# Performance work log

Hardware: AMD Instinct MI355X
Metric: run time of the kernel (lower is better)

Reference implementation:

```python
import jax, jax.numpy as jnp
import numpy as np
from jax import lax

H_IMG = 224
NUM_HEADS = 8
EPS = 1e-5


def setup_inputs() -> dict:
    key = jax.random.key(0)
    ks = jax.random.split(key, 16)
    C, Dff = 256, 512
    conv_s = 1.0 / np.sqrt(C * 9)
    lin_s = 1.0 / np.sqrt(C)
    lin2_s = 1.0 / np.sqrt(Dff)
    inp = {
        'lidar': jax.random.normal(ks[0], (2, C, H_IMG, H_IMG), jnp.float32),
        'image': jax.random.normal(ks[1], (2, C, H_IMG, H_IMG), jnp.float32),
        'cl_w': jax.random.normal(ks[2], (C, C, 3, 3), jnp.float32) * conv_s,
        'cl_b': jnp.zeros((C,), jnp.float32),
        'bnl_g': jnp.ones((C,), jnp.float32), 'bnl_b': jnp.zeros((C,), jnp.float32),
        'bnl_m': jnp.zeros((C,), jnp.float32), 'bnl_v': jnp.ones((C,), jnp.float32),
        'ci_w': jax.random.normal(ks[3], (C, C, 3, 3), jnp.float32) * conv_s,
        'ci_b': jnp.zeros((C,), jnp.float32),
        'bni_g': jnp.ones((C,), jnp.float32), 'bni_b': jnp.zeros((C,), jnp.float32),
        'bni_m': jnp.zeros((C,), jnp.float32), 'bni_v': jnp.ones((C,), jnp.float32),
        'qw': jax.random.normal(ks[4], (C, C), jnp.float32) * lin_s,
        'qb': jnp.zeros((C,), jnp.float32),
        'kw': jax.random.normal(ks[5], (C, C), jnp.float32) * lin_s,
        'kb': jnp.zeros((C,), jnp.float32),
        'vw': jax.random.normal(ks[6], (C, C), jnp.float32) * lin_s,
        'vb': jnp.zeros((C,), jnp.float32),
        'ow': jax.random.normal(ks[7], (C, C), jnp.float32) * lin_s,
        'ob': jnp.zeros((C,), jnp.float32),
        'ln1_g': jnp.ones((C,), jnp.float32), 'ln1_b': jnp.zeros((C,), jnp.float32),
        'w1': jax.random.normal(ks[8], (C, Dff), jnp.float32) * lin_s,
        'b1': jnp.zeros((Dff,), jnp.float32),
        'w2': jax.random.normal(ks[9], (Dff, C), jnp.float32) * lin2_s,
        'b2': jnp.zeros((C,), jnp.float32),
        'ln2_g': jnp.ones((C,), jnp.float32), 'ln2_b': jnp.zeros((C,), jnp.float32),
        'op_w': jax.random.normal(ks[10], (C, C, 1, 1), jnp.float32) * lin_s,
        'op_b': jnp.zeros((C,), jnp.float32),
        'sp_w': jax.random.normal(ks[11], (C, C, 1, 1), jnp.float32) * lin_s,
        'sp_b': jnp.zeros((C,), jnp.float32),
    }
    return inp


def _conv(x, w, b, stride, pad):
    y = lax.conv_general_dilated(x, w, (stride, stride), ((pad, pad), (pad, pad)),
                                 dimension_numbers=('NCHW', 'OIHW', 'NCHW'))
    return y + b[None, :, None, None]


def _bn(x, g, b, m, v):  # eval-mode BatchNorm2d
    inv = g * lax.rsqrt(v + EPS)
    return x * inv[None, :, None, None] + (b - m * inv)[None, :, None, None]


def _ln(x, g, b):
    mu = jnp.mean(x, -1, keepdims=True)
    var = jnp.mean(jnp.square(x - mu), -1, keepdims=True)
    return (x - mu) * lax.rsqrt(var + EPS) * g + b


def reference(lidar, image, cl_w, cl_b, bnl_g, bnl_b, bnl_m, bnl_v,
              ci_w, ci_b, bni_g, bni_b, bni_m, bni_v,
              qw, qb, kw, kb, vw, vb, ow, ob, ln1_g, ln1_b,
              w1, b1, w2, b2, ln2_g, ln2_b, op_w, op_b, sp_w, sp_b):
    B, C, H, W = lidar.shape
    # spatial compression (stride-4 conv + BN + ReLU)
    lc = jax.nn.relu(_bn(_conv(lidar, cl_w, cl_b, 4, 1), bnl_g, bnl_b, bnl_m, bnl_v))
    ic = jax.nn.relu(_bn(_conv(image, ci_w, ci_b, 4, 1), bni_g, bni_b, bni_m, bni_v))
    _, Ch, Hc, Wc = lc.shape
    N = Hc * Wc
    lseq = lc.reshape(B, Ch, N).transpose(0, 2, 1)  # (B,N,C)
    iseq = ic.reshape(B, Ch, N).transpose(0, 2, 1)

    # cross-attention (lidar queries, image keys/values)
    h, d = NUM_HEADS, Ch // NUM_HEADS
    scale = d ** -0.5
    Q = (lseq @ qw + qb).reshape(B, N, h, d).transpose(0, 2, 1, 3)
    K = (iseq @ kw + kb).reshape(B, N, h, d).transpose(0, 2, 1, 3)
    V = (iseq @ vw + vb).reshape(B, N, h, d).transpose(0, 2, 1, 3)
    scores = jnp.einsum('bhqd,bhkd->bhqk', Q, K) * scale
    attn = jax.nn.softmax(scores, axis=-1)
    ctx = jnp.einsum('bhqk,bhkd->bhqd', attn, V)
    attn_out = ctx.transpose(0, 2, 1, 3).reshape(B, N, Ch) @ ow + ob

    x = _ln(lseq + attn_out, ln1_g, ln1_b)
    ffn = jax.nn.relu(x @ w1 + b1) @ w2 + b2
    x = _ln(x + ffn, ln2_g, ln2_b)

    oc = x.transpose(0, 2, 1).reshape(B, Ch, Hc, Wc)
    up = jax.image.resize(oc, (B, Ch, H, W), method='bilinear')  # align_corners=False semantics
    out = _conv(up, op_w, op_b, 1, 0) + _conv(lidar, sp_w, sp_b, 1, 0)
    return out
```

## Files before the change

kernel.cpp:

```cpp
#include <hip/hip_runtime.h>
#include <hip/hip_bf16.h>

typedef __bf16 bf16;
typedef __attribute__((ext_vector_type(8))) __bf16 bf16x8;
typedef __attribute__((ext_vector_type(4))) __bf16 bf16x4;
typedef __attribute__((ext_vector_type(4))) float f32x4;
typedef __attribute__((ext_vector_type(4))) unsigned int u32x4;

#define LN_EPS 1e-5f

__device__ __forceinline__ void gload16(const void* g, void* l) {
  __builtin_amdgcn_global_load_lds(
      (__attribute__((address_space(1))) void*)g,
      (__attribute__((address_space(3))) void*)l, 16, 0, 0);
}

__device__ __forceinline__ unsigned pk2(float a, float b) {
  unsigned ua = __builtin_bit_cast(unsigned short, (bf16)a);
  unsigned ub = __builtin_bit_cast(unsigned short, (bf16)b);
  return ua | (ub << 16);
}

__device__ __forceinline__ float fexp2(float x) {
  float r;
  asm("v_exp_f32 %0, %1" : "=v"(r) : "v"(x));
  return r;
}


__global__ void bn_prep2_k(const float* cb0, const float* g0, const float* b0,
                           const float* m0, const float* v0, float* sc0, float* sh0,
                           const float* cb1, const float* g1, const float* b1,
                           const float* m1, const float* v1, float* sc1, float* sh1,
                           float* zp) {
  int c = threadIdx.x;
  bool z = blockIdx.x != 0;
  const float* cb = z ? cb1 : cb0;
  const float* g = z ? g1 : g0;
  const float* bb = z ? b1 : b0;
  const float* m = z ? m1 : m0;
  const float* v = z ? v1 : v0;
  float* sc = z ? sc1 : sc0;
  float* sh = z ? sh1 : sh0;
  float s = g[c] * rsqrtf(v[c] + LN_EPS);
  sc[c] = s;
  sh[c] = (cb[c] - m[c]) * s + bb[c];
  if (blockIdx.x == 0) zp[c] = 0.f;
}

__global__ void t_cvt4_k(const float* a0, const float* a1, const float* a2,
                         const float* a3, bf16* o0, bf16* o1, bf16* o2, bf16* o3) {
  __shared__ float tile[32][33];
  int z = blockIdx.z;
  const float* in = z == 0 ? a0 : z == 1 ? a1 : z == 2 ? a2 : a3;
  bf16* out = z == 0 ? o0 : z == 1 ? o1 : z == 2 ? o2 : o3;
  int c0 = blockIdx.x * 32, r0 = blockIdx.y * 32;
  int tx = threadIdx.x, ty = threadIdx.y;
  for (int yy = ty; yy < 32; yy += 8)
    tile[yy][tx] = in[(long)(r0 + yy) * 256 + c0 + tx];
  __syncthreads();
  for (int yy = ty; yy < 32; yy += 8)
    out[(long)(c0 + yy) * 256 + r0 + tx] = (bf16)tile[tx][yy];
}

__global__ void t_cvt_k(const float* __restrict__ in, bf16* __restrict__ out,
                        int R, int Cc) {
  __shared__ float tile[32][33];
  int c0 = blockIdx.x * 32, r0 = blockIdx.y * 32;
  int tx = threadIdx.x, ty = threadIdx.y;
  for (int yy = ty; yy < 32; yy += 8)
    tile[yy][tx] = in[(long)(r0 + yy) * Cc + c0 + tx];
  __syncthreads();
  for (int yy = ty; yy < 32; yy += 8)
    out[(long)(c0 + yy) * R + r0 + tx] = (bf16)tile[tx][yy];
}

__global__ void cvt2_k(const float* a0, const float* a1, bf16* o0, bf16* o1, int n) {
  const float* in = blockIdx.y ? a1 : a0;
  bf16* out = blockIdx.y ? o1 : o0;
  int i = (blockIdx.x * 256 + threadIdx.x) * 4;
  if (i < n) {
    float4 v = *(const float4*)(in + i);
    bf16x4 o = {(bf16)v.x, (bf16)v.y, (bf16)v.z, (bf16)v.w};
    *(bf16x4*)(out + i) = o;
  }
}

__global__ void wprep_k(const float* w0, const float* w1, bf16* o0, bf16* o1) {
  const float* w = blockIdx.y ? w1 : w0;
  bf16* o = blockIdx.y ? o1 : o0;
  int idx = blockIdx.x * 256 + threadIdx.x;
  int co = idx / 2304, r = idx - co * 2304;
  int k9 = r >> 8, ci = r & 255;
  o[idx] = (bf16)w[(co * 256 + ci) * 9 + k9];
}

__global__ __launch_bounds__(256) void t_in_k(const float* __restrict__ lid,
                                              const float* __restrict__ img,
                                              bf16* __restrict__ lidT,
                                              bf16* __restrict__ imgT) {
  int z = blockIdx.z;
  int b = z & 1;
  const float* in = (z < 2) ? lid : img;
  bf16* out = (z < 2) ? lidT : imgT;
  long p0 = (long)blockIdx.x * 64;
  int c0 = blockIdx.y * 64;
  __shared__ unsigned tile[64 * 36];
  int t = threadIdx.x;
  const float* ib = in + (long)b * 256 * 50176;
  bf16* ob = out + (long)b * 50176 * 256;
  int q = t & 15;
  int cp = t >> 4;
#pragma unroll
  for (int pp = 0; pp < 2; ++pp) {
    int ch = pp * 32 + cp * 2;
    const float* s = ib + (long)(c0 + ch) * 50176 + p0 + q * 4;
    float4 a = *(const float4*)s;
    float4 bv = *(const float4*)(s + 50176);
    unsigned wv[4] = {pk2(a.x, bv.x), pk2(a.y, bv.y), pk2(a.z, bv.z),
                      pk2(a.w, bv.w)};
    int g_log = pp * 4 + (cp >> 2);
    int colp = ((g_log ^ (q & 7)) << 2) | (cp & 3);
#pragma unroll
    for (int j = 0; j < 4; ++j)
      tile[(q * 4 + j) * 36 + colp] = wv[j];
  }
  __syncthreads();
  int px = t >> 3;
  int c8 = t & 7;
#pragma unroll
  for (int pp = 0; pp < 2; ++pp) {
    int p = pp * 32 + px;
    int colp = (c8 ^ ((p >> 2) & 7)) << 2;
    u32x4 vv = *(const u32x4*)&tile[p * 36 + colp];
    *(u32x4*)(ob + (p0 + p) * 256 + c0 + c8 * 8) = vv;
  }
}

__global__ void t_v_k(const bf16* __restrict__ V, bf16* __restrict__ Vt) {
  __shared__ bf16 tile[32][33];
  int b = blockIdx.z;
  int n0 = blockIdx.x * 32, c0 = blockIdx.y * 32;
  int tx = threadIdx.x, ty = threadIdx.y;
  for (int yy = ty; yy < 32; yy += 8)
    tile[yy][tx] = V[(long)(b * 3136 + n0 + yy) * 256 + c0 + tx];
  __syncthreads();
  for (int yy = ty; yy < 32; yy += 8)
    Vt[(long)(b * 256 + c0 + yy) * 3136 + n0 + tx] = tile[tx][yy];
}

__global__ void ln_k(const float* __restrict__ in, const float* __restrict__ g,
                     const float* __restrict__ bb, float* __restrict__ outf,
                     bf16* __restrict__ outb) {
  int w = threadIdx.x >> 6, l = threadIdx.x & 63;
  long row = (long)blockIdx.x * 4 + w;
  float4 v = *(const float4*)(in + row * 256 + l * 4);
  float s = v.x + v.y + v.z + v.w;
  for (int m = 1; m < 64; m <<= 1) s += __shfl_xor(s, m);
  float mu = s * (1.0f / 256.0f);
  float dx = v.x - mu, dy = v.y - mu, dz = v.z - mu, dw = v.w - mu;
  float q = dx * dx + dy * dy + dz * dz + dw * dw;
  for (int m = 1; m < 64; m <<= 1) q += __shfl_xor(q, m);
  float rstd = rsqrtf(q * (1.0f / 256.0f) + LN_EPS);
  int c = l * 4;
  float y0 = dx * rstd * g[c] + bb[c];
  float y1 = dy * rstd * g[c + 1] + bb[c + 1];
  float y2 = dz * rstd * g[c + 2] + bb[c + 2];
  float y3 = dw * rstd * g[c + 3] + bb[c + 3];
  if (outf) {
    float4 o = {y0, y1, y2, y3};
    *(float4*)(outf + row * 256 + c) = o;
  }
  bf16x4 ob = {(bf16)y0, (bf16)y1, (bf16)y2, (bf16)y3};
  *(bf16x4*)(outb + row * 256 + c) = ob;
}

__global__ __launch_bounds__(256) void upadd_k(float* __restrict__ out,
                                               const float* __restrict__ oc2T) {
  int id = blockIdx.x * 256 + threadIdx.x;
  int xq = id % 56;
  int rest = id / 56;
  int y = rest % 224;
  int rest2 = rest / 224;
  float4 v = *(float4*)(out + (long)id * 4);
  int ry = y & 3;
  int y0 = (y >> 2) - 1 + (ry >> 1);
  float wy = (ry == 0) ? 0.625f : (ry == 1) ? 0.875f : (ry == 2) ? 0.125f : 0.375f;
  int y0c = y0 > 0 ? y0 : 0, y1c = (y0 + 1) < 55 ? (y0 + 1) : 55;
  const float* base = oc2T + (long)rest2 * 3136;
  const float* r0 = base + y0c * 56;
  const float* r1 = base + y1c * 56;
  int xm = xq > 0 ? xq - 1 : 0;
  int xp = xq < 55 ? xq + 1 : 55;
  float a0 = r0[xm], a1 = r0[xq], a2 = r0[xp];
  float b0 = r1[xm], b1 = r1[xq], b2 = r1[xp];
  float t0 = 0.375f * a0 + 0.625f * a1;
  float t1 = 0.125f * a0 + 0.875f * a1;
  float t2 = 0.875f * a1 + 0.125f * a2;
  float t3 = 0.625f * a1 + 0.375f * a2;
  float u0 = 0.375f * b0 + 0.625f * b1;
  float u1 = 0.125f * b0 + 0.875f * b1;
  float u2 = 0.875f * b1 + 0.125f * b2;
  float u3 = 0.625f * b1 + 0.375f * b2;
  float iw = 1.f - wy;
  v.x += iw * t0 + wy * u0;
  v.y += iw * t1 + wy * u1;
  v.z += iw * t2 + wy * u2;
  v.w += iw * t3 + wy * u3;
  *(float4*)(out + (long)id * 4) = v;
}

struct ConvJob {
  const bf16* inT;
  const bf16* wT;
  const float* scale;
  const float* shift;
  bf16* out;
};

__global__ __launch_bounds__(256) void convgemm_k(ConvJob j0, ConvJob j1,
                                                  const bf16* zp) {
  const ConvJob jb = blockIdx.z ? j1 : j0;
  __shared__ bf16 lA[64 * 64];
  __shared__ bf16 lB[64 * 64];
  const int tid = threadIdx.x;
  const int w = tid >> 6, l = tid & 63;
  const int l15 = l & 15;
  const int m0 = blockIdx.x * 64;
  const int n0 = blockIdx.y * 64;
  const int mw = (w >> 1) * 32, nw = (w & 1) * 32;
  f32x4 acc[2][2] = {};
  const int srow = w * 8 + (l >> 3);
  const int kc8 = (l & 7) * 8;
  long rb[2];
  int voy[2], vox[2];
#pragma unroll
  for (int p = 0; p < 2; ++p) {
    int m = m0 + srow + p * 32;
    int b = m / 3136;
    int mm = m - b * 3136;
    int oy = mm / 56, ox = mm - oy * 56;
    rb[p] = ((long)b * 50176 + (long)(4 * oy - 1) * 224 + (4 * ox - 1)) * 256 + kc8;
    voy[p] = oy;
    vox[p] = ox;
  }
  const bf16* Bb = jb.wT + (long)(n0 + srow) * 2304 + kc8;
  bf16* lAp = &lA[srow * 64 + kc8];
  bf16* lBp = &lB[srow * 64 + kc8];
  const bf16* zsrc = zp + kc8;
#pragma unroll
  for (int st = 0; st < 36; ++st) {
    const int k9 = st >> 2, ci0 = (st & 3) * 64;
    const int ky = k9 / 3, kx = k9 - 3 * ky;
    const long koff = (long)(ky * 224 + kx) * 256 + ci0;
#pragma unroll
    for (int p = 0; p < 2; ++p) {
      bool ok = (voy[p] > 0 || ky > 0) && (vox[p] > 0 || kx > 0);
      const bf16* src = ok ? jb.inT + rb[p] + koff : zsrc;
      gload16(src, lAp + p * 32 * 64);
    }
    gload16(Bb + st * 64, lBp);
    gload16(Bb + 32 * 2304 + st * 64, lBp + 32 * 64);
    __syncthreads();
    const int kq = (l >> 4) * 8;
#pragma unroll
    for (int kk = 0; kk < 64; kk += 32) {
      bf16x8 af[2], bfv[2];
#pragma unroll
      for (int i = 0; i < 2; ++i)
        af[i] = *(const bf16x8*)&lA[(mw + i * 16 + l15) * 64 + kk + kq];
#pragma unroll
      for (int j = 0; j < 2; ++j)
        bfv[j] = *(const bf16x8*)&lB[(nw + j * 16 + l15) * 64 + kk + kq];
#pragma unroll
      for (int i = 0; i < 2; ++i)
#pragma unroll
        for (int j = 0; j < 2; ++j)
          acc[i][j] = __builtin_amdgcn_mfma_f32_16x16x32_bf16(af[i], bfv[j],
                                                              acc[i][j], 0, 0, 0);
    }
    __syncthreads();
  }
#pragma unroll
  for (int i = 0; i < 2; ++i)
#pragma unroll
    for (int j = 0; j < 2; ++j)
#pragma unroll
      for (int r = 0; r < 4; ++r) {
        const long row = m0 + mw + i * 16 + (l >> 4) * 4 + r;
        const long col = n0 + nw + j * 16 + l15;
        float v = fmaxf(acc[i][j][r] * jb.scale[col] + jb.shift[col], 0.f);
        jb.out[row * 256 + col] = (bf16)v;
      }
}


struct EpiParams {
  float* out0;
  bf16* out1;
  const float* v0;
  const float* res;
  const bf16* resb;
  int ldc;
  float mul;
};

struct GemmJob {
  const bf16* A;
  const bf16* Bt;
  EpiParams ep;
};

struct GemmJobs3 {
  GemmJob j[3];
};

enum { EPI_QKV = 0, EPI_BIAS_RELU_BF16 = 1, EPI_BIAS_ADD = 2,
       EPI_BIAS_ADDB = 3, EPI_ROWB_F32 = 4, EPI_SPADD = 5 };

template <int EPI, int BM, int BN>
__global__ __launch_bounds__(256) void gemm_bt(GemmJobs3 jobs, int K) {
  const GemmJob jb = jobs.j[blockIdx.z];
  const bf16* __restrict__ A = jb.A;
  const bf16* __restrict__ Bt = jb.Bt;
  const EpiParams ep = jb.ep;
  constexpr int MI = (BM == 128 && BN == 128) ? 4 : 2;
  constexpr int NJ = (BN == 128) ? 4 : 2;
  __shared__ bf16 lA[BM * 64];
  __shared__ bf16 lB[BN * 64];
  const int tid = threadIdx.x;
  const int w = tid >> 6, l = tid & 63;
  const int l15 = l & 15;
  const long m0 = (long)blockIdx.x * BM;
  const long n0 = (long)blockIdx.y * BN;
  const int mw = (BM == 128) ? ((BN == 128) ? (w >> 1) * 64 : w * 32)
                             : (w >> 1) * 32;
  const int nw = (BN == 128) ? (w & 1) * 64 : ((BM == 128) ? 0 : (w & 1) * 32);
  f32x4 acc[MI][NJ] = {};
  const int srow = w * 8 + (l >> 3);
  const int kc8 = (l & 7) * 8;
  const bf16* Ab = A + (m0 + srow) * (long)K + kc8;
  const bf16* Bb = Bt + (n0 + srow) * (long)K + kc8;
  bf16* lAp = &lA[srow * 64 + kc8];
  bf16* lBp = &lB[srow * 64 + kc8];
  for (int k0 = 0; k0 < K; k0 += 64) {
#pragma unroll
    for (int p = 0; p < BM / 32; ++p)
      gload16(Ab + (long)p * 32 * K + k0, lAp + p * 32 * 64);
#pragma unroll
    for (int p = 0; p < BN / 32; ++p)
      gload16(Bb + (long)p * 32 * K + k0, lBp + p * 32 * 64);
    __syncthreads();
    const int kq = (l >> 4) * 8;
#pragma unroll
    for (int kk = 0; kk < 64; kk += 32) {
      bf16x8 af[MI], bfv[NJ];
#pragma unroll
      for (int i = 0; i < MI; ++i)
        af[i] = *(const bf16x8*)&lA[(mw + i * 16 + l15) * 64 + kk + kq];
#pragma unroll
      for (int j = 0; j < NJ; ++j)
        bfv[j] = *(const bf16x8*)&lB[(nw + j * 16 + l15) * 64 + kk + kq];
#pragma unroll
      for (int i = 0; i < MI; ++i)
#pragma unroll
        for (int j = 0; j < NJ; ++j)
          acc[i][j] = __builtin_amdgcn_mfma_f32_16x16x32_bf16(af[i], bfv[j],
                                                              acc[i][j], 0, 0, 0);
    }
    __syncthreads();
  }
  const int ldc = ep.ldc;
#pragma unroll
  for (int i = 0; i < MI; ++i)
#pragma unroll
    for (int j = 0; j < NJ; ++j)
#pragma unroll
      for (int r = 0; r < 4; ++r) {
        const long row = m0 + mw + i * 16 + (l >> 4) * 4 + r;
        const long col = n0 + nw + j * 16 + l15;
        float v = acc[i][j][r];
        if constexpr (EPI == EPI_QKV) {
          ep.out1[row * ldc + col] = (bf16)((v + ep.v0[col]) * ep.mul);
        } else if constexpr (EPI == EPI_BIAS_RELU_BF16) {
          ep.out1[row * ldc + col] = (bf16)fmaxf(v + ep.v0[col], 0.f);
        } else if constexpr (EPI == EPI_BIAS_ADD) {
          ep.out0[row * ldc + col] = v + ep.v0[col] + ep.res[row * ldc + col];
        } else if constexpr (EPI == EPI_BIAS_ADDB) {
          ep.out0[row * ldc + col] =
              v + ep.v0[col] + (float)ep.resb[row * ldc + col];
        } else if constexpr (EPI == EPI_ROWB_F32) {
          ep.out0[row * ldc + col] = v + ep.v0[row];
        } else {
          ep.out0[row * ldc + col] = v + ep.v0[row];
        }
      }
}

__global__ __launch_bounds__(256) void flash_k(const bf16* __restrict__ Qg,
                                               const bf16* __restrict__ Kg,
                                               const bf16* __restrict__ Vt,
                                               bf16* __restrict__ ctx) {
  const int w = threadIdx.x >> 6, l = threadIdx.x & 63;
  const int fid = blockIdx.x;
  const int grp = (fid & 7) * 2 + ((fid >> 3) / 49);
  const int qt = (fid >> 3) % 49;
  const int b = grp >> 3, h = grp & 7;
  const int N = 3136;
  const int l15 = l & 15, g = l >> 4;
  const int q0 = (qt * 4 + w) * 16;
  const int kperm = 8 * (l15 >> 2) + (l15 & 3);
  __shared__ bf16 lds[2][4][512];

  bf16x8 qf = *(const bf16x8*)(Qg + ((long)(b * N + q0 + l15)) * 256 + h * 32 + g * 8);
  const bf16* Kb_ = Kg + ((long)b * N) * 256 + h * 32;
  const bf16* Vb_ = Vt + ((long)(b * 256 + h * 32)) * 3136;
  const long kOffA = (long)kperm * 256 + g * 8;
  const long kOffB = (long)(kperm + 4) * 256 + g * 8;
  const long vOff0 = (long)l15 * 3136 + g * 8;
  const long vOff1 = (long)(16 + l15) * 3136 + g * 8;

  f32x4 o0 = {}, o1 = {};
  float ls = 0.f;

  auto stage = [&](int buf, int kt) {
    const bf16* kp = Kb_ + (long)kt * 32 * 256;
    const bf16* vp = Vb_ + kt * 32;
    if (w == 0)
      gload16(kp + kOffA, &lds[buf][0][l * 8]);
    else if (w == 1)
      gload16(kp + kOffB, &lds[buf][1][l * 8]);
    else if (w == 2)
      gload16(vp + vOff0, &lds[buf][2][l * 8]);
    else
      gload16(vp + vOff1, &lds[buf][3][l * 8]);
  };

  stage(0, 0);
  __syncthreads();
  int cur = 0;
  for (int kt = 0; kt < 98; ++kt) {
    if (kt < 97) stage(cur ^ 1, kt + 1);
    bf16x8 kf0 = *(const bf16x8*)&lds[cur][0][l * 8];
    bf16x8 kf1 = *(const bf16x8*)&lds[cur][1][l * 8];
    bf16x8 vf0 = *(const bf16x8*)&lds[cur][2][l * 8];
    bf16x8 vf1 = *(const bf16x8*)&lds[cur][3][l * 8];
    f32x4 z = {};
    f32x4 s0 = __builtin_amdgcn_mfma_f32_16x16x32_bf16(kf0, qf, z, 0, 0, 0);
    f32x4 s1 = __builtin_amdgcn_mfma_f32_16x16x32_bf16(kf1, qf, z, 0, 0, 0);
    float p0 = fexp2(s0[0]), p1 = fexp2(s0[1]), p2 = fexp2(s0[2]), p3 = fexp2(s0[3]);
    float p4 = fexp2(s1[0]), p5 = fexp2(s1[1]), p6 = fexp2(s1[2]), p7 = fexp2(s1[3]);
    ls += ((p0 + p1) + (p2 + p3)) + ((p4 + p5) + (p6 + p7));
    u32x4 fp;
    fp[0] = pk2(p0, p1);
    fp[1] = pk2(p2, p3);
    fp[2] = pk2(p4, p5);
    fp[3] = pk2(p6, p7);
    bf16x8 pf = __builtin_bit_cast(bf16x8, fp);
    o0 = __builtin_amdgcn_mfma_f32_16x16x32_bf16(vf0, pf, o0, 0, 0, 0);
    o1 = __builtin_amdgcn_mfma_f32_16x16x32_bf16(vf1, pf, o1, 0, 0, 0);
    __syncthreads();
    cur ^= 1;
  }
  ls += __shfl_xor(ls, 16);
  ls += __shfl_xor(ls, 32);
  float inv = 1.0f / ls;
  long base = ((long)(b * N + q0 + l15)) * 256 + h * 32;
  bf16x4 ov0 = {(bf16)(o0[0] * inv), (bf16)(o0[1] * inv),
                (bf16)(o0[2] * inv), (bf16)(o0[3] * inv)};
  bf16x4 ov1 = {(bf16)(o1[0] * inv), (bf16)(o1[1] * inv),
                (bf16)(o1[2] * inv), (bf16)(o1[3] * inv)};
  *(bf16x4*)(ctx + base + g * 4) = ov0;
  *(bf16x4*)(ctx + base + 16 + g * 4) = ov1;
}


extern "C" void kernel_launch(void* const* d_in, const int* in_sizes, int n_in,
                              void* d_out, int out_size, void* d_ws, size_t ws_size,
                              hipStream_t stream) {
  const float* lidar = (const float*)d_in[0];
  const float* image = (const float*)d_in[1];
  const float* cl_w = (const float*)d_in[2];
  const float* cl_b = (const float*)d_in[3];
  const float* bnl_g = (const float*)d_in[4];
  const float* bnl_b = (const float*)d_in[5];
  const float* bnl_m = (const float*)d_in[6];
  const float* bnl_v = (const float*)d_in[7];
  const float* ci_w = (const float*)d_in[8];
  const float* ci_b = (const float*)d_in[9];
  const float* bni_g = (const float*)d_in[10];
  const float* bni_b = (const float*)d_in[11];
  const float* bni_m = (const float*)d_in[12];
  const float* bni_v = (const float*)d_in[13];
  const float* qw = (const float*)d_in[14];
  const float* qb = (const float*)d_in[15];
  const float* kw = (const float*)d_in[16];
  const float* kb = (const float*)d_in[17];
  const float* vw = (const float*)d_in[18];
  const float* vb = (const float*)d_in[19];
  const float* ow = (const float*)d_in[20];
  const float* ob = (const float*)d_in[21];
  const float* ln1_g = (const float*)d_in[22];
  const float* ln1_b = (const float*)d_in[23];
  const float* w1 = (const float*)d_in[24];
  const float* b1 = (const float*)d_in[25];
  const float* w2 = (const float*)d_in[26];
  const float* b2 = (const float*)d_in[27];
  const float* ln2_g = (const float*)d_in[28];
  const float* ln2_b = (const float*)d_in[29];
  const float* op_w = (const float*)d_in[30];
  const float* op_b = (const float*)d_in[31];
  const float* sp_w = (const float*)d_in[32];
  const float* sp_b = (const float*)d_in[33];
  float* out = (float*)d_out;

  char* ws = (char*)d_ws;
  bf16* lidT = (bf16*)ws;
  bf16* imgT = (bf16*)(ws + 51380224);
  char* ov = ws + 51380224;
  bf16* Qb = (bf16*)(ov + 0);
  bf16* Kb = (bf16*)(ov + 3211264);
  bf16* Vb = (bf16*)(ov + 6422528);
  bf16* Vt = (bf16*)(ov + 9633792);
  bf16* ctx = (bf16*)(ov + 12845056);
  bf16* x_b = (bf16*)(ov + 16056320);
  float* tmp1 = (float*)(ov + 19267584);
  float* x_f = (float*)(ov + 25690112);
  bf16* hmid = (bf16*)(ov + 32112640);
  float* oc2T = (float*)(ov + 38535168);
  size_t off = 102760448;
  auto carve = [&](size_t bytes) {
    void* p = ws + off;
    off += (bytes + 255) & ~(size_t)255;
    return p;
  };
  bf16* lseq_b = (bf16*)carve(3211264);
  bf16* iseq_b = (bf16*)carve(3211264);
  bf16* qwT = (bf16*)carve(131072);
  bf16* kwT = (bf16*)carve(131072);
  bf16* vwT = (bf16*)carve(131072);
  bf16* owT = (bf16*)carve(131072);
  bf16* w1t = (bf16*)carve(262144);
  bf16* w2t = (bf16*)carve(262144);
  bf16* clwT = (bf16*)carve(1179648);
  bf16* ciwT = (bf16*)carve(1179648);
  bf16* opwB = (bf16*)carve(131072);
  bf16* spwB = (bf16*)carve(131072);
  float* scale_l = (float*)carve(1024);
  float* shift_l = (float*)carve(1024);
  float* scale_i = (float*)carve(1024);
  float* shift_i = (float*)carve(1024);
  float* zp = (float*)carve(1024);
  float* tmp2 = tmp1;
  bf16* x2_pad = (bf16*)(void*)x_f;

  dim3 b32x8(32, 8);
  const float qscale = 0.17677669529663687f * 1.4426950408889634f;

  bn_prep2_k<<<2, 256, 0, stream>>>(cl_b, bnl_g, bnl_b, bnl_m, bnl_v, scale_l, shift_l,
                                    ci_b, bni_g, bni_b, bni_m, bni_v, scale_i, shift_i,
                                    zp);
  t_cvt4_k<<<dim3(8, 8, 4), b32x8, 0, stream>>>(qw, kw, vw, ow, qwT, kwT, vwT, owT);
  t_cvt_k<<<dim3(16, 8), b32x8, 0, stream>>>(w1, w1t, 256, 512);
  t_cvt_k<<<dim3(8, 16), b32x8, 0, stream>>>(w2, w2t, 512, 256);
  cvt2_k<<<dim3(64, 2), 256, 0, stream>>>(op_w, sp_w, opwB, spwB, 65536);
  wprep_k<<<dim3(2304, 2), 256, 0, stream>>>(cl_w, ci_w, clwT, ciwT);

  t_in_k<<<dim3(784, 4, 4), 256, 0, stream>>>(lidar, image, lidT, imgT);

  {
    ConvJob j0{lidT, clwT, scale_l, shift_l, lseq_b};
    ConvJob j1{imgT, ciwT, scale_i, shift_i, iseq_b};
    convgemm_k<<<dim3(98, 4, 2), 256, 0, stream>>>(j0, j1, (const bf16*)zp);
  }
  {
    GemmJobs3 js{};
    js.j[0] = {lseq_b, qwT, {nullptr, Qb, qb, nullptr, nullptr, 256, qscale}};
    js.j[1] = {iseq_b, kwT, {nullptr, Kb, kb, nullptr, nullptr, 256, 1.f}};
    js.j[2] = {iseq_b, vwT, {nullptr, Vb, vb, nullptr, nullptr, 256, 1.f}};
    gemm_bt<EPI_QKV, 64, 64><<<dim3(98, 4, 3), 256, 0, stream>>>(js, 256);
  }
  t_v_k<<<dim3(98, 8, 2), b32x8, 0, stream>>>(Vb, Vt);
  flash_k<<<dim3(784), 256, 0, stream>>>(Qb, Kb, Vt, ctx);
  {
    GemmJobs3 js{};
    js.j[0] = {ctx, owT, {tmp1, nullptr, ob, nullptr, lseq_b, 256, 1.f}};
    gemm_bt<EPI_BIAS_ADDB, 64, 64><<<dim3(98, 4, 1), 256, 0, stream>>>(js, 256);
  }
  ln_k<<<1568, 256, 0, stream>>>(tmp1, ln1_g, ln1_b, x_f, x_b);
  {
    GemmJobs3 js{};
    js.j[0] = {x_b, w1t, {nullptr, hmid, b1, nullptr, nullptr, 512, 1.f}};
    gemm_bt<EPI_BIAS_RELU_BF16, 64, 64><<<dim3(98, 8, 1), 256, 0, stream>>>(js, 256);
  }
  {
    GemmJobs3 js{};
    js.j[0] = {hmid, w2t, {tmp2, nullptr, b2, x_f, nullptr, 256, 1.f}};
    gemm_bt<EPI_BIAS_ADD, 64, 64><<<dim3(98, 4, 1), 256, 0, stream>>>(js, 512);
  }
  ln_k<<<1568, 256, 0, stream>>>(tmp2, ln2_g, ln2_b, nullptr, x2_pad);
  {
    GemmJobs3 js{};
    js.j[0] = {opwB, x2_pad, {oc2T, nullptr, op_b, nullptr, nullptr, 3136, 1.f}};
    js.j[1] = {opwB, x2_pad + (long)3136 * 256,
               {oc2T + (long)256 * 3136, nullptr, op_b, nullptr, nullptr, 3136, 1.f}};
    gemm_bt<EPI_ROWB_F32, 64, 64><<<dim3(4, 49, 2), 256, 0, stream>>>(js, 256);
  }
  {
    GemmJobs3 js{};
    js.j[0] = {spwB, lidT, {out, nullptr, sp_b, nullptr, nullptr, 50176, 1.f}};
    js.j[1] = {spwB, lidT + (long)50176 * 256,
               {out + (long)256 * 50176, nullptr, sp_b, nullptr, nullptr, 50176, 1.f}};
    gemm_bt<EPI_SPADD, 128, 128><<<dim3(2, 392, 2), 256, 0, stream>>>(js, 256);
  }
  upadd_k<<<25088, 256, 0, stream>>>(out, oc2T);
}
```

Measured before the change: 346.9 us.

## Fuse bilinear upsample-add into final GEMM epilogue and enlarge input transpose tiles

The separate upadd_k pass, which reread and rewrote the full 2x256x224x224 fp32 output, is removed. Its bilinear interpolation of oc2T is now computed in the epilogue of the 1x1 skip-projection GEMM. That GEMM moves from 128x128 to 64x64 tiles. The input transpose kernel now uses 128x128 tiles with a padded, unswizzled LDS layout instead of 64x64 XOR-swizzled tiles. The cost is four gathered oc2T loads and extra index arithmetic per output element, smaller GEMM tiles with less reuse, and possible LDS bank conflicts in the transpose.

```diff
diff --git a/kernel.cpp b/kernel.cpp
--- a/kernel.cpp
+++ b/kernel.cpp
@@ -103,36 +103,33 @@
   int b = z & 1;
   const float* in = (z < 2) ? lid : img;
   bf16* out = (z < 2) ? lidT : imgT;
-  long p0 = (long)blockIdx.x * 64;
-  int c0 = blockIdx.y * 64;
-  __shared__ unsigned tile[64 * 36];
+  long p0 = (long)blockIdx.x * 128;
+  int c0 = blockIdx.y * 128;
+  __shared__ unsigned tile[128 * 68];
   int t = threadIdx.x;
   const float* ib = in + (long)b * 256 * 50176;
   bf16* ob = out + (long)b * 50176 * 256;
-  int q = t & 15;
-  int cp = t >> 4;
-#pragma unroll
-  for (int pp = 0; pp < 2; ++pp) {
-    int ch = pp * 32 + cp * 2;
-    const float* s = ib + (long)(c0 + ch) * 50176 + p0 + q * 4;
+  int q = t & 31;
+  int cp = t >> 5;
+#pragma unroll
+  for (int pp = 0; pp < 8; ++pp) {
+    int chl = pp * 16 + cp * 2;
+    const float* s = ib + (long)(c0 + chl) * 50176 + p0 + q * 4;
     float4 a = *(const float4*)s;
     float4 bv = *(const float4*)(s + 50176);
     unsigned wv[4] = {pk2(a.x, bv.x), pk2(a.y, bv.y), pk2(a.z, bv.z),
                       pk2(a.w, bv.w)};
-    int g_log = pp * 4 + (cp >> 2);
-    int colp = ((g_log ^ (q & 7)) << 2) | (cp & 3);
+    int c = pp * 8 + cp;
 #pragma unroll
     for (int j = 0; j < 4; ++j)
-      tile[(q * 4 + j) * 36 + colp] = wv[j];
+      tile[(q * 4 + j) * 68 + c] = wv[j];
   }
   __syncthreads();
-  int px = t >> 3;
-  int c8 = t & 7;
-#pragma unroll
-  for (int pp = 0; pp < 2; ++pp) {
-    int p = pp * 32 + px;
-    int colp = (c8 ^ ((p >> 2) & 7)) << 2;
-    u32x4 vv = *(const u32x4*)&tile[p * 36 + colp];
+  int c8 = t & 15;
+#pragma unroll
+  for (int pp = 0; pp < 8; ++pp) {
+    int p = pp * 16 + (t >> 4);
+    u32x4 vv = *(const u32x4*)&tile[p * 68 + c8 * 4];
     *(u32x4*)(ob + (p0 + p) * 256 + c0 + c8 * 8) = vv;
   }
 }
@@ -175,41 +172,6 @@
   *(bf16x4*)(outb + row * 256 + c) = ob;
 }
 
-__global__ __launch_bounds__(256) void upadd_k(float* __restrict__ out,
-                                               const float* __restrict__ oc2T) {
-  int id = blockIdx.x * 256 + threadIdx.x;
-  int xq = id % 56;
-  int rest = id / 56;
-  int y = rest % 224;
-  int rest2 = rest / 224;
-  float4 v = *(float4*)(out + (long)id * 4);
-  int ry = y & 3;
-  int y0 = (y >> 2) - 1 + (ry >> 1);
-  float wy = (ry == 0) ? 0.625f : (ry == 1) ? 0.875f : (ry == 2) ? 0.125f : 0.375f;
-  int y0c = y0 > 0 ? y0 : 0, y1c = (y0 + 1) < 55 ? (y0 + 1) : 55;
-  const float* base = oc2T + (long)rest2 * 3136;
-  const float* r0 = base + y0c * 56;
-  const float* r1 = base + y1c * 56;
-  int xm = xq > 0 ? xq - 1 : 0;
-  int xp = xq < 55 ? xq + 1 : 55;
-  float a0 = r0[xm], a1 = r0[xq], a2 = r0[xp];
-  float b0 = r1[xm], b1 = r1[xq], b2 = r1[xp];
-  float t0 = 0.375f * a0 + 0.625f * a1;
-  float t1 = 0.125f * a0 + 0.875f * a1;
-  float t2 = 0.875f * a1 + 0.125f * a2;
-  float t3 = 0.625f * a1 + 0.375f * a2;
-  float u0 = 0.375f * b0 + 0.625f * b1;
-  float u1 = 0.125f * b0 + 0.875f * b1;
-  float u2 = 0.875f * b1 + 0.125f * b2;
-  float u3 = 0.625f * b1 + 0.375f * b2;
-  float iw = 1.f - wy;
-  v.x += iw * t0 + wy * u0;
-  v.y += iw * t1 + wy * u1;
-  v.z += iw * t2 + wy * u2;
-  v.w += iw * t3 + wy * u3;
-  *(float4*)(out + (long)id * 4) = v;
-}
-
 struct ConvJob {
   const bf16* inT;
   const bf16* wT;
@@ -316,7 +278,7 @@
 };
 
 enum { EPI_QKV = 0, EPI_BIAS_RELU_BF16 = 1, EPI_BIAS_ADD = 2,
-       EPI_BIAS_ADDB = 3, EPI_ROWB_F32 = 4, EPI_SPADD = 5 };
+       EPI_BIAS_ADDB = 3, EPI_ROWB_F32 = 4, EPI_FINAL2 = 5 };
 
 template <int EPI, int BM, int BN>
 __global__ __launch_bounds__(256) void gemm_bt(GemmJobs3 jobs, int K) {
@@ -392,7 +354,24 @@
         } else if constexpr (EPI == EPI_ROWB_F32) {
           ep.out0[row * ldc + col] = v + ep.v0[row];
         } else {
-          ep.out0[row * ldc + col] = v + ep.v0[row];
+          int colp = (int)col;
+          int y = colp / 224, x = colp - y * 224;
+          int ry = y & 3, rx = x & 3;
+          int y0 = (y >> 2) - 1 + (ry >> 1);
+          int x0 = (x >> 2) - 1 + (rx >> 1);
+          float wy = (ry == 0) ? 0.625f : (ry == 1) ? 0.875f : (ry == 2) ? 0.125f : 0.375f;
+          float wx = (rx == 0) ? 0.625f : (rx == 1) ? 0.875f : (rx == 2) ? 0.125f : 0.375f;
+          int y0c = y0 > 0 ? y0 : 0, y1c = (y0 + 1) < 55 ? (y0 + 1) : 55;
+          int x0c = x0 > 0 ? x0 : 0, x1c = (x0 + 1) < 55 ? (x0 + 1) : 55;
+          int co = (int)row;
+          const float* ocr = ep.res + (long)co * 3136;
+          float v00 = ocr[y0c * 56 + x0c];
+          float v01 = ocr[y0c * 56 + x1c];
+          float v10 = ocr[y1c * 56 + x0c];
+          float v11 = ocr[y1c * 56 + x1c];
+          float up = (1.f - wy) * ((1.f - wx) * v00 + wx * v01) +
+                     wy * ((1.f - wx) * v10 + wx * v11);
+          ep.out0[row * ldc + col] = v + ep.v0[co] + up;
         }
       }
 }
@@ -566,7 +545,7 @@
   cvt2_k<<<dim3(64, 2), 256, 0, stream>>>(op_w, sp_w, opwB, spwB, 65536);
   wprep_k<<<dim3(2304, 2), 256, 0, stream>>>(cl_w, ci_w, clwT, ciwT);
 
-  t_in_k<<<dim3(784, 4, 4), 256, 0, stream>>>(lidar, image, lidT, imgT);
+  t_in_k<<<dim3(392, 2, 4), 256, 0, stream>>>(lidar, image, lidT, imgT);
 
   {
     ConvJob j0{lidT, clwT, scale_l, shift_l, lseq_b};
@@ -608,10 +587,10 @@
   }
   {
     GemmJobs3 js{};
-    js.j[0] = {spwB, lidT, {out, nullptr, sp_b, nullptr, nullptr, 50176, 1.f}};
+    js.j[0] = {spwB, lidT, {out, nullptr, sp_b, oc2T, nullptr, 50176, 1.f}};
     js.j[1] = {spwB, lidT + (long)50176 * 256,
-               {out + (long)256 * 50176, nullptr, sp_b, nullptr, nullptr, 50176, 1.f}};
-    gemm_bt<EPI_SPADD, 128, 128><<<dim3(2, 392, 2), 256, 0, stream>>>(js, 256);
-  }
-  upadd_k<<<25088, 256, 0, stream>>>(out, oc2T);
-}
+               {out + (long)256 * 50176, nullptr, sp_b,
+                oc2T + (long)256 * 3136, nullptr, 50176, 1.f}};
+    gemm_bt<EPI_FINAL2, 64, 64><<<dim3(4, 784, 2), 256, 0, stream>>>(js, 256);
+  }
+}
```

New measurement: 323.5 us. -6.7%, faster.
